# Kernel tuning notes

Measured on AMD Instinct MI355X. Metric: run time of the kernel, lower is better.

Reference implementation:

```python
import jax, jax.numpy as jnp
import numpy as np

B, S, D, H = 1, 4096, 1024, 16
HD = D // H  # head_size = 64

def setup_inputs() -> dict:
    key = jax.random.key(0)
    ks = jax.random.split(key, 9)
    scale = 1.0 / np.sqrt(D)
    return {
        "x": jax.random.normal(ks[0], (B, S, D), jnp.float32),
        "Wq": jax.random.normal(ks[1], (D, D), jnp.float32) * scale,
        "bq": jax.random.normal(ks[2], (D,), jnp.float32) * 0.01,
        "Wk": jax.random.normal(ks[3], (D, D), jnp.float32) * scale,
        "bk": jax.random.normal(ks[4], (D,), jnp.float32) * 0.01,
        "Wv": jax.random.normal(ks[5], (D, D), jnp.float32) * scale,
        "bv": jax.random.normal(ks[6], (D,), jnp.float32) * 0.01,
        "Wo": jax.random.normal(ks[7], (D, D), jnp.float32) * scale,
        "bo": jax.random.normal(ks[8], (D,), jnp.float32) * 0.01,
    }

def _split_heads(t):
    # (B, S, D) -> (B, H, S, HD)
    return t.reshape(B, S, H, HD).transpose(0, 2, 1, 3)

def reference(x, Wq, bq, Wk, bk, Wv, bv, Wo, bo):
    q = _split_heads(x @ Wq + bq)
    k = _split_heads(x @ Wk + bk)
    v = _split_heads(x @ Wv + bv)
    # scores: (B, H, S, S), materialized as in the original naive attention
    scores = jnp.einsum('bhqd,bhkd->bhqk', q, k) / jnp.sqrt(jnp.asarray(HD, q.dtype))
    causal = jnp.tril(jnp.ones((S, S), dtype=bool))  # tril mask, broadcast over (B, H)
    scores = jnp.where(causal[None, None], scores, jnp.asarray(-1e9, scores.dtype))
    attn = jax.nn.softmax(scores, axis=-1)
    out = jnp.einsum('bhqk,bhkd->bhqd', attn, v)  # (B, H, S, HD)
    out = out.transpose(0, 2, 1, 3).reshape(B, S, D)  # combine heads
    return out @ Wo + bo
```

## Files before the change

### kernel.cpp

```cpp
#include <hip/hip_runtime.h>

#define SEQ 4096
#define DM  1024
#define NH  16
#define HDIM 64

typedef unsigned short u16;
typedef unsigned int   u32;
typedef __bf16 bf16x8 __attribute__((ext_vector_type(8)));
typedef float f32x4 __attribute__((ext_vector_type(4)));

__device__ __forceinline__ float bf2f(u16 u) {
    unsigned v = ((unsigned)u) << 16;
    float f;
    __builtin_memcpy(&f, &v, 4);
    return f;
}
__device__ __forceinline__ u16 f2bf(float f) {
    unsigned u;
    __builtin_memcpy(&u, &f, 4);
    return (u16)((u + 0x7fffu + ((u >> 16) & 1u)) >> 16);
}
__device__ __forceinline__ u32 bfpack(float a, float b) {
    u32 ua, ub;
    __builtin_memcpy(&ua, &a, 4);
    __builtin_memcpy(&ub, &b, 4);
    return ((ua + 0x8000u) >> 16) | ((ub + 0x8000u) & 0xffff0000u);
}

typedef const __attribute__((address_space(1))) unsigned int gas_uint;
typedef __attribute__((address_space(3))) unsigned int las_uint;
__device__ __forceinline__ void gld16(const u16* g, u16* l) {
    __builtin_amdgcn_global_load_lds((gas_uint*)g, (las_uint*)l, 16, 0, 0);
}

__device__ __forceinline__ f32x4 mfma16(bf16x8 a, bf16x8 b, f32x4 c) {
    return __builtin_amdgcn_mfma_f32_16x16x32_bf16(a, b, c, 0, 0, 0);
}

__global__ __launch_bounds__(256) void detect_k(const u16* __restrict__ w,
                                                int* __restrict__ flags) {
    __shared__ float red[256];
    const int t = threadIdx.x;
    float mx = 0.f;
    for (int i = t; i < 4096; i += 256) {
        float v = fabsf(bf2f(w[i]));
        if (v < 3e38f) mx = fmaxf(mx, v);
    }
    red[t] = mx;
    __syncthreads();
    for (int s = 128; s > 0; s >>= 1) {
        if (t < s) red[t] = fmaxf(red[t], red[t + s]);
        __syncthreads();
    }
    if (t == 0) {
        flags[0] = (red[0] > 1e4f) ? 1 : 0;
        flags[1] = 0;
    }
}

__global__ __launch_bounds__(256) void prep_w(const void* w0, const void* w1,
                                              const void* w2, const void* w3,
                                              const void* b0, const void* b1,
                                              const void* b2, const void* b3,
                                              u16* __restrict__ wt,
                                              u16* __restrict__ b_dst,
                                              const int* __restrict__ flags) {
    __shared__ u16 tile[32][33];
    const int f = flags[0];
    const int z = blockIdx.z;
    const void* win[4] = {w0, w1, w2, w3};
    const void* bin[4] = {b0, b1, b2, b3};
    const void* in = win[z];
    u16* out = wt + (size_t)z * DM * DM;
    const float scale = (z == 0) ? 0.125f : 1.0f;

    const int bx = blockIdx.x * 32;
    const int by = blockIdx.y * 32;
    const int tx = threadIdx.x & 31;
    const int ty = threadIdx.x >> 5;
#pragma unroll
    for (int i = ty; i < 32; i += 8) {
        size_t idx = (size_t)(by + i) * DM + bx + tx;
        float v = f ? ((const float*)in)[idx] : bf2f(((const u16*)in)[idx]);
        tile[i][tx] = f2bf(v * scale);
    }
    __syncthreads();
#pragma unroll
    for (int i = ty; i < 32; i += 8) out[(size_t)(bx + i) * DM + by + tx] = tile[tx][i];

    if (blockIdx.x == 0 && blockIdx.y == 0) {
        const void* bi = bin[z];
        for (int i = threadIdx.x; i < DM; i += 256) {
            float v = f ? ((const float*)bi)[i] : bf2f(((const u16*)bi)[i]);
            b_dst[z * DM + i] = f2bf(v * scale);
        }
    }
}

__global__ __launch_bounds__(256) void cvt_x8(const void* __restrict__ src,
                                              u16* __restrict__ dst,
                                              const int* __restrict__ flags) {
    const size_t i = ((size_t)blockIdx.x * 256 + threadIdx.x) * 8;
    if (flags[0]) {
        const float4* s4 = (const float4*)((const float*)src + i);
        float4 a = s4[0], b = s4[1];
        uint4 o;
        o.x = bfpack(a.x, a.y);
        o.y = bfpack(a.z, a.w);
        o.z = bfpack(b.x, b.y);
        o.w = bfpack(b.z, b.w);
        *(uint4*)(dst + i) = o;
    } else {
        *(uint4*)(dst + i) = *(const uint4*)((const u16*)src + i);
    }
}

__global__ __launch_bounds__(256, 2) void gemm128(const u16* __restrict__ A,
                                                  const u16* __restrict__ Bt,
                                                  const u16* __restrict__ bias,
                                                  void* __restrict__ C,
                                                  int M, int N, int K,
                                                  const int* __restrict__ flags) {
    __shared__ u16 As[128 * 32];
    __shared__ u16 Bs[128 * 32];
    const int f    = flags[0];
    const int tid  = threadIdx.x;
    const int lane = tid & 63;
    const int w    = tid >> 6;
    const int m    = lane & 15;
    const int quad = lane >> 4;
    const int wr   = w >> 1;
    const int wc   = w & 1;
    const int mb = blockIdx.x * 128;
    const int nb = blockIdx.y * 128;

    f32x4 acc[4][4] = {};

    for (int kb = 0; kb < K; kb += 32) {
        __syncthreads();
#pragma unroll
        for (int i = 0; i < 2; ++i) {
            const int Lb = i * 256 + w * 64;
            const int L  = Lb + lane;
            const int row = L >> 2, cb = L & 3;
            gld16(&A[(size_t)(mb + row) * K + kb + cb * 8], &As[Lb * 8]);
            gld16(&Bt[(size_t)(nb + row) * K + kb + cb * 8], &Bs[Lb * 8]);
        }
        __syncthreads();

        bf16x8 af[4];
#pragma unroll
        for (int mt = 0; mt < 4; ++mt)
            af[mt] = *(const bf16x8*)&As[(wr * 64 + mt * 16 + m) * 32 + quad * 8];
#pragma unroll
        for (int ct = 0; ct < 4; ++ct) {
            bf16x8 bfr = *(const bf16x8*)&Bs[(wc * 64 + ct * 16 + m) * 32 + quad * 8];
#pragma unroll
            for (int mt = 0; mt < 4; ++mt)
                acc[mt][ct] = mfma16(af[mt], bfr, acc[mt][ct]);
        }
    }

#pragma unroll
    for (int ct = 0; ct < 4; ++ct) {
        float bv = bf2f(bias[nb + wc * 64 + ct * 16 + m]);
#pragma unroll
        for (int mt = 0; mt < 4; ++mt) {
#pragma unroll
            for (int r = 0; r < 4; ++r) {
                int row = mb + wr * 64 + mt * 16 + quad * 4 + r;
                size_t idx = (size_t)row * N + nb + wc * 64 + ct * 16 + m;
                float v = acc[mt][ct][r] + bv;
                if (f) ((float*)C)[idx] = v;
                else   ((u16*)C)[idx]   = f2bf(v);
            }
        }
    }
}

__global__ __launch_bounds__(256) void vt_k(const u16* __restrict__ qkv,
                                            u16* __restrict__ Vt) {
    __shared__ u16 T[64][72];
    const int st = blockIdx.x;
    const int h  = blockIdx.y;
    const int t  = threadIdx.x;
    const int sl = t >> 2, c = t & 3;
    const u16* src = &qkv[(size_t)(st * 64 + sl) * 3072 + 2048 + h * 64 + c * 16];
    *(uint4*)&T[sl][c * 16]     = *(const uint4*)src;
    *(uint4*)&T[sl][c * 16 + 8] = *(const uint4*)(src + 8);
    __syncthreads();
    const int dl = t >> 2, c2 = t & 3;
    u16 tmp[16];
#pragma unroll
    for (int i = 0; i < 16; ++i) tmp[i] = T[c2 * 16 + i][dl];
    u16* dst = &Vt[(size_t)(h * 64 + dl) * SEQ + st * 64 + c2 * 16];
    *(uint4*)dst       = *(const uint4*)&tmp[0];
    *(uint4*)(dst + 8) = *(const uint4*)&tmp[8];
}

__global__ __launch_bounds__(256, 2) void attn_k(const u16* __restrict__ QKV,
                                                 const u16* __restrict__ Vt,
                                                 u16* __restrict__ O) {
    __shared__ u16 Ks[2][64 * 64];
    __shared__ u16 Vs[2][64 * 64];
    __shared__ u16 Ps[4][32 * 72];

    const int tid  = threadIdx.x;
    const int lane = tid & 63;
    const int w    = tid >> 6;
    const int m    = lane & 15;
    const int quad = lane >> 4;

    const int d    = blockIdx.x;
    const int half = d >> 8;
    const int c    = d & 255;
    const int qt   = half ? ((c >> 3) & 31) : (31 - ((c >> 3) & 31));
    const int h    = ((c & 7) << 1) + half;
    const int hc   = h * HDIM;

    const int qbw    = qt * 128 + w * 32;
    const int dkt    = qbw >> 6;
    const int kt_end = 2 * qt + 1;

    const int l3 = lane >> 3;
    const int cx = ((lane & 7) ^ l3) * 8;
    const int xr8 = m & 7;

    bf16x8 qf[2][2];
#pragma unroll
    for (int mt = 0; mt < 2; ++mt)
#pragma unroll
        for (int kh = 0; kh < 2; ++kh)
            qf[mt][kh] = *(const bf16x8*)&QKV[(size_t)(qbw + mt * 16 + m) * 3072 + hc + kh * 32 + quad * 8];

    f32x4 o_acc[2][4] = {};
    f32x4 l_part[2] = {};

#pragma unroll
    for (int i = 0; i < 2; ++i) {
        const int rsub = i * 8 + l3;
        gld16(&QKV[(size_t)(4 * rsub + w) * 3072 + 1024 + hc + cx], &Ks[0][(w * 16 + i * 8) * 64]);
        gld16(&Vt[(size_t)(hc + w * 16 + rsub) * SEQ + cx],          &Vs[0][(w * 16 + i * 8) * 64]);
    }

    for (int kt = 0; kt <= kt_end; ++kt) {
        const int cur = kt & 1;
        __syncthreads();

        if (kt < kt_end) {
            const int nb = 1 - cur;
            const int nkt = kt + 1;
#pragma unroll
            for (int i = 0; i < 2; ++i) {
                const int rsub = i * 8 + l3;
                gld16(&QKV[(size_t)(nkt * 64 + 4 * rsub + w) * 3072 + 1024 + hc + cx],
                      &Ks[nb][(w * 16 + i * 8) * 64]);
                gld16(&Vt[(size_t)(hc + w * 16 + rsub) * SEQ + nkt * 64 + cx],
                      &Vs[nb][(w * 16 + i * 8) * 64]);
            }
        }

        if (kt > dkt) continue;

        const u16* ksb = Ks[cur];
        const u16* vsb = Vs[cur];

        f32x4 sc[2][4];
#pragma unroll
        for (int ct = 0; ct < 4; ++ct) {
            const int rb = (ct * 16 + m) * 64;
            bf16x8 k0 = *(const bf16x8*)&ksb[rb + ((quad ^ xr8) * 8)];
            bf16x8 k1 = *(const bf16x8*)&ksb[rb + (((quad + 4) ^ xr8) * 8)];
#pragma unroll
            for (int mt = 0; mt < 2; ++mt) {
                f32x4 a = {};
                a = mfma16(qf[mt][0], k0, a);
                a = mfma16(qf[mt][1], k1, a);
                sc[mt][ct] = a;
            }
        }

        if (kt < dkt) {
#pragma unroll
            for (int mt = 0; mt < 2; ++mt)
#pragma unroll
                for (int ct = 0; ct < 4; ++ct)
#pragma unroll
                    for (int r = 0; r < 4; ++r)
                        sc[mt][ct][r] = __expf(sc[mt][ct][r]);
        } else {
#pragma unroll
            for (int mt = 0; mt < 2; ++mt)
#pragma unroll
                for (int ct = 0; ct < 4; ++ct) {
                    const int j = kt * 64 + 4 * m + ct;
#pragma unroll
                    for (int r = 0; r < 4; ++r) {
                        const int i2 = qbw + mt * 16 + quad * 4 + r;
                        float p = __expf(sc[mt][ct][r]);
                        sc[mt][ct][r] = (j > i2) ? 0.f : p;
                    }
                }
        }

#pragma unroll
        for (int mt = 0; mt < 2; ++mt)
#pragma unroll
            for (int r = 0; r < 4; ++r)
                l_part[mt][r] += sc[mt][0][r] + sc[mt][1][r] + sc[mt][2][r] + sc[mt][3][r];

        u16* psw = (u16*)&Ps[w][0];
#pragma unroll
        for (int mt = 0; mt < 2; ++mt)
#pragma unroll
            for (int r = 0; r < 4; ++r) {
                uint2 val;
                val.x = bfpack(sc[mt][0][r], sc[mt][1][r]);
                val.y = bfpack(sc[mt][2][r], sc[mt][3][r]);
                *(uint2*)&psw[(mt * 16 + quad * 4 + r) * 72 + 4 * m] = val;
            }

        bf16x8 pf0[2], pf1[2];
#pragma unroll
        for (int mt = 0; mt < 2; ++mt) {
            pf0[mt] = *(const bf16x8*)&psw[(mt * 16 + m) * 72 + quad * 8];
            pf1[mt] = *(const bf16x8*)&psw[(mt * 16 + m) * 72 + 32 + quad * 8];
        }
#pragma unroll
        for (int ct = 0; ct < 4; ++ct) {
            const int rb = (ct * 16 + m) * 64;
            bf16x8 v0 = *(const bf16x8*)&vsb[rb + ((quad ^ xr8) * 8)];
            bf16x8 v1 = *(const bf16x8*)&vsb[rb + (((quad + 4) ^ xr8) * 8)];
#pragma unroll
            for (int mt = 0; mt < 2; ++mt) {
                o_acc[mt][ct] = mfma16(pf0[mt], v0, o_acc[mt][ct]);
                o_acc[mt][ct] = mfma16(pf1[mt], v1, o_acc[mt][ct]);
            }
        }
    }

#pragma unroll
    for (int off = 1; off < 16; off <<= 1)
#pragma unroll
        for (int mt = 0; mt < 2; ++mt)
#pragma unroll
            for (int r = 0; r < 4; ++r)
                l_part[mt][r] += __shfl_xor(l_part[mt][r], off, 64);

#pragma unroll
    for (int mt = 0; mt < 2; ++mt) {
        float inv[4];
#pragma unroll
        for (int r = 0; r < 4; ++r) inv[r] = 1.0f / l_part[mt][r];
#pragma unroll
        for (int ct = 0; ct < 4; ++ct)
#pragma unroll
            for (int r = 0; r < 4; ++r) {
                int row = qbw + mt * 16 + quad * 4 + r;
                O[(size_t)row * DM + hc + ct * 16 + m] = f2bf(o_acc[mt][ct][r] * inv[r]);
            }
    }
}

extern "C" void kernel_launch(void* const* d_in, const int* in_sizes, int n_in,
                              void* d_out, int out_size, void* d_ws, size_t ws_size,
                              hipStream_t stream) {
    (void)in_sizes; (void)n_in; (void)out_size; (void)ws_size;

    u16* ws    = (u16*)d_ws;
    int* flags = (int*)d_ws;
    u16* xc    = ws + 64;
    u16* Vt_g  = xc;
    u16* Wtqkv = xc + (size_t)SEQ * DM;
    u16* Wto   = Wtqkv + (size_t)3 * DM * DM;
    u16* bqkv  = Wto + (size_t)DM * DM;
    u16* boc   = bqkv + 3 * DM;
    u16* qkv   = boc + DM;
    u16* ab    = qkv + (size_t)SEQ * 3 * DM;

    detect_k<<<1, 256, 0, stream>>>((const u16*)d_in[1], flags);

    prep_w<<<dim3(DM / 32, DM / 32, 4), 256, 0, stream>>>(
        d_in[1], d_in[3], d_in[5], d_in[7],
        d_in[2], d_in[4], d_in[6], d_in[8],
        Wtqkv, bqkv, flags);

    cvt_x8<<<SEQ * DM / 2048, 256, 0, stream>>>(d_in[0], xc, flags);

    gemm128<<<dim3(SEQ / 128, 3 * DM / 128), 256, 0, stream>>>(
        xc, Wtqkv, bqkv, qkv, SEQ, 3 * DM, DM, flags + 1);

    vt_k<<<dim3(SEQ / 64, NH), 256, 0, stream>>>(qkv, Vt_g);

    attn_k<<<dim3(512), 256, 0, stream>>>(qkv, Vt_g, ab);

    gemm128<<<dim3(SEQ / 128, DM / 128), 256, 0, stream>>>(
        ab, Wto, boc, d_out, SEQ, DM, DM, flags);
}
```

Measured before the change: 248.1 us.

## Use atomic work queue with split-K for long causal attention tiles

Replaces the static per-block causal attention grid with a persistent kernel that pulls tasks from an atomic counter. The longest query tiles (the upper half) are split into two key ranges whose unnormalised partial outputs and row sums go to scratch slots, and a separate merge kernel sums and normalises them. The aim is to balance the triangular causal workload across CUs and shorten the tail. The cost is an extra launch, bf16 rounding of partial sums, and extra scratch traffic. The old static kernel is kept as a fallback when the workspace is too small.

```diff
diff --git a/kernel.cpp b/kernel.cpp
--- a/kernel.cpp
+++ b/kernel.cpp
@@ -56,6 +56,7 @@
     if (t == 0) {
         flags[0] = (red[0] > 1e4f) ? 1 : 0;
         flags[1] = 0;
+        flags[8] = 0;
     }
 }
 
@@ -199,55 +200,271 @@
     *(uint4*)(dst + 8) = *(const uint4*)&tmp[8];
 }
 
-__global__ __launch_bounds__(256, 2) void attn_k(const u16* __restrict__ QKV,
-                                                 const u16* __restrict__ Vt,
-                                                 u16* __restrict__ O) {
+__global__ __launch_bounds__(256, 2) void attn_queue(const u16* __restrict__ QKV,
+                                                     const u16* __restrict__ Vt,
+                                                     u16* __restrict__ O,
+                                                     u16* __restrict__ slotA,
+                                                     u16* __restrict__ slotB,
+                                                     float* __restrict__ lA,
+                                                     float* __restrict__ lB,
+                                                     int* __restrict__ counter) {
     __shared__ u16 Ks[2][64 * 64];
     __shared__ u16 Vs[2][64 * 64];
     __shared__ u16 Ps[4][32 * 72];
+    __shared__ int task_s;
 
     const int tid  = threadIdx.x;
     const int lane = tid & 63;
     const int w    = tid >> 6;
     const int m    = lane & 15;
     const int quad = lane >> 4;
-
+    const int l3   = lane >> 3;
+    const int cx   = ((lane & 7) ^ l3) * 8;
+    const int xr8  = m & 7;
+
+    while (true) {
+        if (tid == 0) task_s = atomicAdd(counter, 1);
+        __syncthreads();
+        const int t = task_s;
+        if (t >= 768) break;
+
+        int qt, h, k0t, k1t, mode;
+        if (t < 64) {
+            qt = 15 - (t >> 4); h = t & 15; k0t = 0; k1t = 2 * qt + 1; mode = 0;
+        } else if (t < 576) {
+            int u = t - 64;
+            qt = 31 - (u >> 5); h = (u >> 1) & 15;
+            if ((u & 1) == 0) { k0t = 0;      k1t = qt;         mode = 1; }
+            else              { k0t = qt + 1; k1t = 2 * qt + 1; mode = 2; }
+        } else {
+            int u = t - 576;
+            qt = 11 - (u >> 4); h = u & 15; k0t = 0; k1t = 2 * qt + 1; mode = 0;
+        }
+        const int hc  = h * HDIM;
+        const int qbw = qt * 128 + w * 32;
+        const int dkt = qbw >> 6;
+
+        bf16x8 qf[2][2];
+#pragma unroll
+        for (int mt = 0; mt < 2; ++mt)
+#pragma unroll
+            for (int kh = 0; kh < 2; ++kh)
+                qf[mt][kh] = *(const bf16x8*)&QKV[(size_t)(qbw + mt * 16 + m) * 3072 + hc + kh * 32 + quad * 8];
+
+        f32x4 o_acc[2][4] = {};
+        f32x4 l_part[2] = {};
+
+#pragma unroll
+        for (int i = 0; i < 2; ++i) {
+            const int rsub = i * 8 + l3;
+            gld16(&QKV[(size_t)(k0t * 64 + 4 * rsub + w) * 3072 + 1024 + hc + cx],
+                  &Ks[0][(w * 16 + i * 8) * 64]);
+            gld16(&Vt[(size_t)(hc + w * 16 + rsub) * SEQ + k0t * 64 + cx],
+                  &Vs[0][(w * 16 + i * 8) * 64]);
+        }
+
+        for (int kt = k0t; kt <= k1t; ++kt) {
+            const int cur = (kt - k0t) & 1;
+            __syncthreads();
+
+            if (kt < k1t) {
+                const int nb = 1 - cur;
+                const int nkt = kt + 1;
+#pragma unroll
+                for (int i = 0; i < 2; ++i) {
+                    const int rsub = i * 8 + l3;
+                    gld16(&QKV[(size_t)(nkt * 64 + 4 * rsub + w) * 3072 + 1024 + hc + cx],
+                          &Ks[nb][(w * 16 + i * 8) * 64]);
+                    gld16(&Vt[(size_t)(hc + w * 16 + rsub) * SEQ + nkt * 64 + cx],
+                          &Vs[nb][(w * 16 + i * 8) * 64]);
+                }
+            }
+
+            if (kt > dkt) continue;
+
+            const u16* ksb = Ks[cur];
+            const u16* vsb = Vs[cur];
+
+            f32x4 sc[2][4];
+#pragma unroll
+            for (int ct = 0; ct < 4; ++ct) {
+                const int rb = (ct * 16 + m) * 64;
+                bf16x8 k0 = *(const bf16x8*)&ksb[rb + ((quad ^ xr8) * 8)];
+                bf16x8 k1 = *(const bf16x8*)&ksb[rb + (((quad + 4) ^ xr8) * 8)];
+#pragma unroll
+                for (int mt = 0; mt < 2; ++mt) {
+                    f32x4 a = {};
+                    a = mfma16(qf[mt][0], k0, a);
+                    a = mfma16(qf[mt][1], k1, a);
+                    sc[mt][ct] = a;
+                }
+            }
+
+            if (kt < dkt) {
+#pragma unroll
+                for (int mt = 0; mt < 2; ++mt)
+#pragma unroll
+                    for (int ct = 0; ct < 4; ++ct)
+#pragma unroll
+                        for (int r = 0; r < 4; ++r)
+                            sc[mt][ct][r] = __expf(sc[mt][ct][r]);
+            } else {
+#pragma unroll
+                for (int mt = 0; mt < 2; ++mt)
+#pragma unroll
+                    for (int ct = 0; ct < 4; ++ct) {
+                        const int j = kt * 64 + 4 * m + ct;
+#pragma unroll
+                        for (int r = 0; r < 4; ++r) {
+                            const int i2 = qbw + mt * 16 + quad * 4 + r;
+                            float p = __expf(sc[mt][ct][r]);
+                            sc[mt][ct][r] = (j > i2) ? 0.f : p;
+                        }
+                    }
+            }
+
+#pragma unroll
+            for (int mt = 0; mt < 2; ++mt)
+#pragma unroll
+                for (int r = 0; r < 4; ++r)
+                    l_part[mt][r] += sc[mt][0][r] + sc[mt][1][r] + sc[mt][2][r] + sc[mt][3][r];
+
+            u16* psw = (u16*)&Ps[w][0];
+#pragma unroll
+            for (int mt = 0; mt < 2; ++mt)
+#pragma unroll
+                for (int r = 0; r < 4; ++r) {
+                    uint2 val;
+                    val.x = bfpack(sc[mt][0][r], sc[mt][1][r]);
+                    val.y = bfpack(sc[mt][2][r], sc[mt][3][r]);
+                    *(uint2*)&psw[(mt * 16 + quad * 4 + r) * 72 + 4 * m] = val;
+                }
+
+            bf16x8 pf0[2], pf1[2];
+#pragma unroll
+            for (int mt = 0; mt < 2; ++mt) {
+                pf0[mt] = *(const bf16x8*)&psw[(mt * 16 + m) * 72 + quad * 8];
+                pf1[mt] = *(const bf16x8*)&psw[(mt * 16 + m) * 72 + 32 + quad * 8];
+            }
+#pragma unroll
+            for (int ct = 0; ct < 4; ++ct) {
+                const int rb = (ct * 16 + m) * 64;
+                bf16x8 v0 = *(const bf16x8*)&vsb[rb + ((quad ^ xr8) * 8)];
+                bf16x8 v1 = *(const bf16x8*)&vsb[rb + (((quad + 4) ^ xr8) * 8)];
+#pragma unroll
+                for (int mt = 0; mt < 2; ++mt) {
+                    o_acc[mt][ct] = mfma16(pf0[mt], v0, o_acc[mt][ct]);
+                    o_acc[mt][ct] = mfma16(pf1[mt], v1, o_acc[mt][ct]);
+                }
+            }
+        }
+
+#pragma unroll
+        for (int off = 1; off < 16; off <<= 1)
+#pragma unroll
+            for (int mt = 0; mt < 2; ++mt)
+#pragma unroll
+                for (int r = 0; r < 4; ++r)
+                    l_part[mt][r] += __shfl_xor(l_part[mt][r], off, 64);
+
+        if (mode == 0) {
+#pragma unroll
+            for (int mt = 0; mt < 2; ++mt) {
+                float inv[4];
+#pragma unroll
+                for (int r = 0; r < 4; ++r) inv[r] = 1.0f / l_part[mt][r];
+#pragma unroll
+                for (int ct = 0; ct < 4; ++ct)
+#pragma unroll
+                    for (int r = 0; r < 4; ++r) {
+                        int row = qbw + mt * 16 + quad * 4 + r;
+                        O[(size_t)row * DM + hc + ct * 16 + m] = f2bf(o_acc[mt][ct][r] * inv[r]);
+                    }
+            }
+        } else {
+            u16*   slot = (mode == 1) ? slotA : slotB;
+            float* lb   = (mode == 1) ? lA : lB;
+            const int rbase = (qt - 16) * 128 + w * 32;
+#pragma unroll
+            for (int mt = 0; mt < 2; ++mt)
+#pragma unroll
+                for (int ct = 0; ct < 4; ++ct)
+#pragma unroll
+                    for (int r = 0; r < 4; ++r) {
+                        int rl = rbase + mt * 16 + quad * 4 + r;
+                        slot[(size_t)rl * DM + hc + ct * 16 + m] = f2bf(o_acc[mt][ct][r]);
+                    }
+            if (m == 0) {
+#pragma unroll
+                for (int mt = 0; mt < 2; ++mt)
+#pragma unroll
+                    for (int r = 0; r < 4; ++r)
+                        lb[h * 2048 + rbase + mt * 16 + quad * 4 + r] = l_part[mt][r];
+            }
+        }
+    }
+}
+
+__global__ __launch_bounds__(256) void merge_k(const u16* __restrict__ sA,
+                                               const u16* __restrict__ sB,
+                                               const float* __restrict__ lA,
+                                               const float* __restrict__ lB,
+                                               u16* __restrict__ O) {
+    const int gid = blockIdx.x * 256 + threadIdx.x;
+    const int rl = gid >> 7;
+    const int cg = gid & 127;
+    const int h  = cg >> 3;
+    const float inv = 1.0f / (lA[h * 2048 + rl] + lB[h * 2048 + rl]);
+    uint4 va = *(const uint4*)(sA + (size_t)rl * DM + cg * 8);
+    uint4 vb = *(const uint4*)(sB + (size_t)rl * DM + cg * 8);
+    const u16* a16 = (const u16*)&va;
+    const u16* b16 = (const u16*)&vb;
+    u16 oo[8];
+#pragma unroll
+    for (int i = 0; i < 8; ++i) oo[i] = f2bf((bf2f(a16[i]) + bf2f(b16[i])) * inv);
+    *(uint4*)(O + (size_t)(2048 + rl) * DM + cg * 8) = *(const uint4*)&oo[0];
+}
+
+__global__ __launch_bounds__(256, 2) void attn_static(const u16* __restrict__ QKV,
+                                                      const u16* __restrict__ Vt,
+                                                      u16* __restrict__ O) {
+    __shared__ u16 Ks[2][64 * 64];
+    __shared__ u16 Vs[2][64 * 64];
+    __shared__ u16 Ps[4][32 * 72];
+    const int tid  = threadIdx.x;
+    const int lane = tid & 63;
+    const int w    = tid >> 6;
+    const int m    = lane & 15;
+    const int quad = lane >> 4;
     const int d    = blockIdx.x;
     const int half = d >> 8;
     const int c    = d & 255;
     const int qt   = half ? ((c >> 3) & 31) : (31 - ((c >> 3) & 31));
     const int h    = ((c & 7) << 1) + half;
     const int hc   = h * HDIM;
-
     const int qbw    = qt * 128 + w * 32;
     const int dkt    = qbw >> 6;
     const int kt_end = 2 * qt + 1;
-
     const int l3 = lane >> 3;
     const int cx = ((lane & 7) ^ l3) * 8;
     const int xr8 = m & 7;
-
     bf16x8 qf[2][2];
 #pragma unroll
     for (int mt = 0; mt < 2; ++mt)
 #pragma unroll
         for (int kh = 0; kh < 2; ++kh)
             qf[mt][kh] = *(const bf16x8*)&QKV[(size_t)(qbw + mt * 16 + m) * 3072 + hc + kh * 32 + quad * 8];
-
     f32x4 o_acc[2][4] = {};
     f32x4 l_part[2] = {};
-
 #pragma unroll
     for (int i = 0; i < 2; ++i) {
         const int rsub = i * 8 + l3;
         gld16(&QKV[(size_t)(4 * rsub + w) * 3072 + 1024 + hc + cx], &Ks[0][(w * 16 + i * 8) * 64]);
         gld16(&Vt[(size_t)(hc + w * 16 + rsub) * SEQ + cx],          &Vs[0][(w * 16 + i * 8) * 64]);
     }
-
     for (int kt = 0; kt <= kt_end; ++kt) {
         const int cur = kt & 1;
         __syncthreads();
-
         if (kt < kt_end) {
             const int nb = 1 - cur;
             const int nkt = kt + 1;
@@ -260,12 +477,9 @@
                       &Vs[nb][(w * 16 + i * 8) * 64]);
             }
         }
-
         if (kt > dkt) continue;
-
         const u16* ksb = Ks[cur];
         const u16* vsb = Vs[cur];
-
         f32x4 sc[2][4];
 #pragma unroll
         for (int ct = 0; ct < 4; ++ct) {
@@ -280,7 +494,6 @@
                 sc[mt][ct] = a;
             }
         }
-
         if (kt < dkt) {
 #pragma unroll
             for (int mt = 0; mt < 2; ++mt)
@@ -303,13 +516,11 @@
                     }
                 }
         }
-
 #pragma unroll
         for (int mt = 0; mt < 2; ++mt)
 #pragma unroll
             for (int r = 0; r < 4; ++r)
                 l_part[mt][r] += sc[mt][0][r] + sc[mt][1][r] + sc[mt][2][r] + sc[mt][3][r];
-
         u16* psw = (u16*)&Ps[w][0];
 #pragma unroll
         for (int mt = 0; mt < 2; ++mt)
@@ -320,7 +531,6 @@
                 val.y = bfpack(sc[mt][2][r], sc[mt][3][r]);
                 *(uint2*)&psw[(mt * 16 + quad * 4 + r) * 72 + 4 * m] = val;
             }
-
         bf16x8 pf0[2], pf1[2];
 #pragma unroll
         for (int mt = 0; mt < 2; ++mt) {
@@ -339,7 +549,6 @@
             }
         }
     }
-
 #pragma unroll
     for (int off = 1; off < 16; off <<= 1)
 #pragma unroll
@@ -347,7 +556,6 @@
 #pragma unroll
             for (int r = 0; r < 4; ++r)
                 l_part[mt][r] += __shfl_xor(l_part[mt][r], off, 64);
-
 #pragma unroll
     for (int mt = 0; mt < 2; ++mt) {
         float inv[4];
@@ -366,7 +574,7 @@
 extern "C" void kernel_launch(void* const* d_in, const int* in_sizes, int n_in,
                               void* d_out, int out_size, void* d_ws, size_t ws_size,
                               hipStream_t stream) {
-    (void)in_sizes; (void)n_in; (void)out_size; (void)ws_size;
+    (void)in_sizes; (void)n_in; (void)out_size;
 
     u16* ws    = (u16*)d_ws;
     int* flags = (int*)d_ws;
@@ -378,6 +586,12 @@
     u16* boc   = bqkv + 3 * DM;
     u16* qkv   = boc + DM;
     u16* ab    = qkv + (size_t)SEQ * 3 * DM;
+    u16* slotA = ab + (size_t)SEQ * DM;
+    u16* slotB = slotA + (size_t)2048 * DM;
+    float* lAf = (float*)(slotB + (size_t)2048 * DM);
+    float* lBf = lAf + 2048 * NH;
+    const size_t need = ((char*)(lBf + 2048 * NH)) - (char*)d_ws;
+    const bool big = ws_size >= need;
 
     detect_k<<<1, 256, 0, stream>>>((const u16*)d_in[1], flags);
 
@@ -393,7 +607,13 @@
 
     vt_k<<<dim3(SEQ / 64, NH), 256, 0, stream>>>(qkv, Vt_g);
 
-    attn_k<<<dim3(512), 256, 0, stream>>>(qkv, Vt_g, ab);
+    if (big) {
+        attn_queue<<<dim3(512), 256, 0, stream>>>(qkv, Vt_g, ab, slotA, slotB,
+                                                  lAf, lBf, flags + 8);
+        merge_k<<<dim3(1024), 256, 0, stream>>>(slotA, slotB, lAf, lBf, ab);
+    } else {
+        attn_static<<<dim3(512), 256, 0, stream>>>(qkv, Vt_g, ab);
+    }
 
     gemm128<<<dim3(SEQ / 128, DM / 128), 256, 0, stream>>>(
         ab, Wto, boc, d_out, SEQ, DM, DM, flags);
```

Measured after the change: 247.6 us. Within noise of the previous version (-0.2%).

## Split causal attention KV range across two blocks and merge partial outputs

Applied to the files above, without the earlier changes.

Each query tile's causal key range is split into two halves of equal length, each handled by a separate block, so the grid doubles to 1024 blocks and per-block work evens out. Each block writes unnormalized bf16 partial outputs and per-row sums, and a new merge kernel adds the two partials and normalizes them. The softmax exp is also switched to hardware exp2, with log2(e) folded into the Q weight scale. The extra merge pass and the bf16 rounding of unnormalized partials cost added memory traffic and some precision, and dropping the min-blocks launch bound may change register allocation.

```diff
diff --git a/kernel.cpp b/kernel.cpp
--- a/kernel.cpp
+++ b/kernel.cpp
@@ -37,6 +37,8 @@
 __device__ __forceinline__ f32x4 mfma16(bf16x8 a, bf16x8 b, f32x4 c) {
     return __builtin_amdgcn_mfma_f32_16x16x32_bf16(a, b, c, 0, 0, 0);
 }
+
+#define QSCALE 0.18033688011f
 
 __global__ __launch_bounds__(256) void detect_k(const u16* __restrict__ w,
                                                 int* __restrict__ flags) {
@@ -73,7 +75,7 @@
     const void* bin[4] = {b0, b1, b2, b3};
     const void* in = win[z];
     u16* out = wt + (size_t)z * DM * DM;
-    const float scale = (z == 0) ? 0.125f : 1.0f;
+    const float scale = (z == 0) ? QSCALE : 1.0f;
 
     const int bx = blockIdx.x * 32;
     const int by = blockIdx.y * 32;
@@ -199,9 +201,12 @@
     *(uint4*)(dst + 8) = *(const uint4*)&tmp[8];
 }
 
-__global__ __launch_bounds__(256, 2) void attn_k(const u16* __restrict__ QKV,
-                                                 const u16* __restrict__ Vt,
-                                                 u16* __restrict__ O) {
+__global__ __launch_bounds__(256) void attn_split(const u16* __restrict__ QKV,
+                                                  const u16* __restrict__ Vt,
+                                                  u16* __restrict__ ab,
+                                                  u16* __restrict__ slotB,
+                                                  float* __restrict__ lA,
+                                                  float* __restrict__ lB) {
     __shared__ u16 Ks[2][64 * 64];
     __shared__ u16 Vs[2][64 * 64];
     __shared__ u16 Ps[4][32 * 72];
@@ -211,21 +216,23 @@
     const int w    = tid >> 6;
     const int m    = lane & 15;
     const int quad = lane >> 4;
-
-    const int d    = blockIdx.x;
-    const int half = d >> 8;
-    const int c    = d & 255;
-    const int qt   = half ? ((c >> 3) & 31) : (31 - ((c >> 3) & 31));
-    const int h    = ((c & 7) << 1) + half;
+    const int l3   = lane >> 3;
+    const int cx   = ((lane & 7) ^ l3) * 8;
+    const int xr8  = m & 7;
+
+    const int b    = blockIdx.x;
+    const int x    = b & 7;
+    const int j    = b >> 3;
+    const int h    = 2 * x + (j & 1);
+    const int u    = j >> 1;
+    const int qt   = 31 - (u >> 1);
+    const int half = u & 1;
+    const int k0t  = half ? qt + 1 : 0;
+    const int k1t  = half ? 2 * qt + 1 : qt;
     const int hc   = h * HDIM;
 
-    const int qbw    = qt * 128 + w * 32;
-    const int dkt    = qbw >> 6;
-    const int kt_end = 2 * qt + 1;
-
-    const int l3 = lane >> 3;
-    const int cx = ((lane & 7) ^ l3) * 8;
-    const int xr8 = m & 7;
+    const int qbw = qt * 128 + w * 32;
+    const int dkt = qbw >> 6;
 
     bf16x8 qf[2][2];
 #pragma unroll
@@ -240,15 +247,17 @@
 #pragma unroll
     for (int i = 0; i < 2; ++i) {
         const int rsub = i * 8 + l3;
-        gld16(&QKV[(size_t)(4 * rsub + w) * 3072 + 1024 + hc + cx], &Ks[0][(w * 16 + i * 8) * 64]);
-        gld16(&Vt[(size_t)(hc + w * 16 + rsub) * SEQ + cx],          &Vs[0][(w * 16 + i * 8) * 64]);
-    }
-
-    for (int kt = 0; kt <= kt_end; ++kt) {
-        const int cur = kt & 1;
+        gld16(&QKV[(size_t)(k0t * 64 + 4 * rsub + w) * 3072 + 1024 + hc + cx],
+              &Ks[0][(w * 16 + i * 8) * 64]);
+        gld16(&Vt[(size_t)(hc + w * 16 + rsub) * SEQ + k0t * 64 + cx],
+              &Vs[0][(w * 16 + i * 8) * 64]);
+    }
+
+    for (int kt = k0t; kt <= k1t; ++kt) {
+        const int cur = (kt - k0t) & 1;
         __syncthreads();
 
-        if (kt < kt_end) {
+        if (kt < k1t) {
             const int nb = 1 - cur;
             const int nkt = kt + 1;
 #pragma unroll
@@ -288,18 +297,18 @@
                 for (int ct = 0; ct < 4; ++ct)
 #pragma unroll
                     for (int r = 0; r < 4; ++r)
-                        sc[mt][ct][r] = __expf(sc[mt][ct][r]);
+                        sc[mt][ct][r] = __builtin_amdgcn_exp2f(sc[mt][ct][r]);
         } else {
 #pragma unroll
             for (int mt = 0; mt < 2; ++mt)
 #pragma unroll
                 for (int ct = 0; ct < 4; ++ct) {
-                    const int j = kt * 64 + 4 * m + ct;
+                    const int jcol = kt * 64 + 4 * m + ct;
 #pragma unroll
                     for (int r = 0; r < 4; ++r) {
                         const int i2 = qbw + mt * 16 + quad * 4 + r;
-                        float p = __expf(sc[mt][ct][r]);
-                        sc[mt][ct][r] = (j > i2) ? 0.f : p;
+                        float p = __builtin_amdgcn_exp2f(sc[mt][ct][r]);
+                        sc[mt][ct][r] = (jcol > i2) ? 0.f : p;
                     }
                 }
         }
@@ -348,19 +357,43 @@
             for (int r = 0; r < 4; ++r)
                 l_part[mt][r] += __shfl_xor(l_part[mt][r], off, 64);
 
-#pragma unroll
-    for (int mt = 0; mt < 2; ++mt) {
-        float inv[4];
-#pragma unroll
-        for (int r = 0; r < 4; ++r) inv[r] = 1.0f / l_part[mt][r];
+    u16*   dst = half ? slotB : ab;
+    float* lb  = half ? lB : lA;
+#pragma unroll
+    for (int mt = 0; mt < 2; ++mt)
 #pragma unroll
         for (int ct = 0; ct < 4; ++ct)
 #pragma unroll
             for (int r = 0; r < 4; ++r) {
                 int row = qbw + mt * 16 + quad * 4 + r;
-                O[(size_t)row * DM + hc + ct * 16 + m] = f2bf(o_acc[mt][ct][r] * inv[r]);
-            }
-    }
+                dst[(size_t)row * DM + hc + ct * 16 + m] = f2bf(o_acc[mt][ct][r]);
+            }
+    if (m == 0) {
+#pragma unroll
+        for (int mt = 0; mt < 2; ++mt)
+#pragma unroll
+            for (int r = 0; r < 4; ++r)
+                lb[h * SEQ + qbw + mt * 16 + quad * 4 + r] = l_part[mt][r];
+    }
+}
+
+__global__ __launch_bounds__(256) void merge_k(u16* __restrict__ ab,
+                                               const u16* __restrict__ sB,
+                                               const float* __restrict__ lA,
+                                               const float* __restrict__ lB) {
+    const int gid = blockIdx.x * 256 + threadIdx.x;
+    const int rl = gid >> 7;
+    const int cg = gid & 127;
+    const int h  = cg >> 3;
+    const float inv = 1.0f / (lA[h * SEQ + rl] + lB[h * SEQ + rl]);
+    uint4 va = *(const uint4*)(ab + (size_t)rl * DM + cg * 8);
+    uint4 vb = *(const uint4*)(sB + (size_t)rl * DM + cg * 8);
+    const u16* a16 = (const u16*)&va;
+    const u16* b16 = (const u16*)&vb;
+    u16 oo[8];
+#pragma unroll
+    for (int i = 0; i < 8; ++i) oo[i] = f2bf((bf2f(a16[i]) + bf2f(b16[i])) * inv);
+    *(uint4*)(ab + (size_t)rl * DM + cg * 8) = *(const uint4*)&oo[0];
 }
 
 extern "C" void kernel_launch(void* const* d_in, const int* in_sizes, int n_in,
@@ -378,6 +411,9 @@
     u16* boc   = bqkv + 3 * DM;
     u16* qkv   = boc + DM;
     u16* ab    = qkv + (size_t)SEQ * 3 * DM;
+    u16* slotB = ab + (size_t)SEQ * DM;
+    float* lAf = (float*)Wtqkv;
+    float* lBf = lAf + NH * SEQ;
 
     detect_k<<<1, 256, 0, stream>>>((const u16*)d_in[1], flags);
 
@@ -393,7 +429,9 @@
 
     vt_k<<<dim3(SEQ / 64, NH), 256, 0, stream>>>(qkv, Vt_g);
 
-    attn_k<<<dim3(512), 256, 0, stream>>>(qkv, Vt_g, ab);
+    attn_split<<<dim3(1024), 256, 0, stream>>>(qkv, Vt_g, ab, slotB, lAf, lBf);
+
+    merge_k<<<dim3(SEQ * 128 / 256), 256, 0, stream>>>(ab, slotB, lAf, lBf);
 
     gemm128<<<dim3(SEQ / 128, DM / 128), 256, 0, stream>>>(
         ab, Wto, boc, d_out, SEQ, DM, DM, flags);
```

Result: faster. 230.1 us (-7.3%).
